# Performance work log

Hardware: AMD Instinct MI355X
Metric: run time of the kernel (lower is better)

The kernel has to match this reference:

```python
import jax, jax.numpy as jnp
import numpy as np

D_MODEL = 1024
NUM_HEADS = 16
HEAD_DIM = D_MODEL // NUM_HEADS
CLAMP = 1e9


def setup_inputs() -> dict:
    key = jax.random.key(0)
    ks = jax.random.split(key, 5)
    B, S = 2, 2048
    x = jax.random.normal(ks[0], (B, S, D_MODEL), dtype=jnp.float32)
    # causal mask, broadcastable over [B, H, S, S]
    mask = jnp.tril(jnp.ones((S, S), dtype=bool))
    Wqkv = jax.random.normal(ks[1], (D_MODEL, 3 * D_MODEL), dtype=jnp.float32) * (1.0 / np.sqrt(D_MODEL))
    bqkv = jax.random.normal(ks[2], (3 * D_MODEL,), dtype=jnp.float32) * 0.02
    Wo = jax.random.normal(ks[3], (D_MODEL, D_MODEL), dtype=jnp.float32) * (1.0 / np.sqrt(D_MODEL))
    bo = jax.random.normal(ks[4], (D_MODEL,), dtype=jnp.float32) * 0.02
    return {"x": x, "mask": mask, "Wqkv": Wqkv, "bqkv": bqkv, "Wo": Wo, "bo": bo}


def reference(x, mask, Wqkv, bqkv, Wo, bo):
    B, S, _ = x.shape
    qkv = x @ Wqkv + bqkv                               # [B, S, 3*d_model]
    qkv = qkv.reshape(B, S, NUM_HEADS, 3 * HEAD_DIM).transpose(0, 2, 1, 3)  # [B, H, S, 3*hd]
    q, k, v = jnp.split(qkv, 3, axis=-1)                # each [B, H, S, hd]
    scale = 1.0 / np.sqrt(HEAD_DIM)
    scores = jnp.einsum('bhqd,bhkd->bhqk', q, k) * scale  # [B, H, S, S]
    scores = jnp.where(mask, scores, -jnp.inf)
    scores = jnp.clip(scores, -CLAMP, CLAMP)
    attn = jax.nn.softmax(scores, axis=-1)
    values = jnp.einsum('bhqk,bhkd->bhqd', attn, v)     # [B, H, S, hd]
    values = values.transpose(0, 2, 1, 3).reshape(B, S, D_MODEL)
    return values @ Wo + bo
```

## Files before the change

kernel.cpp:

```cpp
#include <hip/hip_runtime.h>
#include <hip/hip_bf16.h>

#define S_LEN 2048
#define NHEAD 16
#define HDIM  64
#define DMODEL 1024

typedef unsigned short u16;
typedef __attribute__((ext_vector_type(8))) short short8;
typedef __attribute__((ext_vector_type(4))) float floatx4;
typedef __attribute__((ext_vector_type(4))) u16 u16x4;

__device__ __forceinline__ u16 f2bf(float f) {
  unsigned u = __builtin_bit_cast(unsigned, f);
  u += 0x7fffu + ((u >> 16) & 1u);
  return (u16)(u >> 16);
}
__device__ __forceinline__ float bf2f(u16 b) {
  unsigned u = ((unsigned)b) << 16;
  return __builtin_bit_cast(float, u);
}
__device__ __forceinline__ void gload_lds16(const void* g, void* l) {
  __builtin_amdgcn_global_load_lds((const __attribute__((address_space(1))) unsigned int*)g,
                                   (__attribute__((address_space(3))) unsigned int*)l,
                                   16, 0, 0);
}
__device__ __forceinline__ int swz(int b) { return b ^ (((b >> 7) & 7) << 4); }

#define MFMA16(a, b, c) __builtin_amdgcn_mfma_f32_16x16x32_bf16(a, b, c, 0, 0, 0)


__global__ __launch_bounds__(256) void k_cast(const float* __restrict__ in,
                                              u16* __restrict__ hi, int n) {
  int i = (blockIdx.x * blockDim.x + threadIdx.x) * 4;
  if (i >= n) return;
  float4 v = *(const float4*)(in + i);
  u16x4 hv = {f2bf(v.x), f2bf(v.y), f2bf(v.z), f2bf(v.w)};
  *(u16x4*)(hi + i) = hv;
}

__global__ void k_transpose(const float* __restrict__ in, u16* __restrict__ oh, int R, int C) {
  __shared__ float t[32][33];
  int c0 = blockIdx.x * 32, r0 = blockIdx.y * 32;
  int tx = threadIdx.x, ty = threadIdx.y;
#pragma unroll
  for (int rr = ty; rr < 32; rr += 8) t[rr][tx] = in[(size_t)(r0 + rr) * C + c0 + tx];
  __syncthreads();
#pragma unroll
  for (int rr = ty; rr < 32; rr += 8) {
    float v = t[tx][rr];
    oh[(size_t)(c0 + rr) * R + r0 + tx] = f2bf(v);
  }
}

__device__ __forceinline__ void gemm_main(const u16* __restrict__ A, const u16* __restrict__ B,
                                          int m0, int n0, floatx4 (&acc)[4][4]) {
  __shared__ __align__(16) u16 sA[2][128 * 32];
  __shared__ __align__(16) u16 sB[2][128 * 32];
  const int tid = threadIdx.x, lane = tid & 63;
  const int wid = tid >> 6, wr = wid >> 1, wc = wid & 1;
  const int cl = lane & 15, hi = lane >> 4;
  const int rmask = ((cl >> 1) & 7) << 4;
  const int aoff = (wr * 4096 + cl * 64 + hi * 16) ^ rmask;
  const int boff = (wc * 4096 + cl * 64 + hi * 16) ^ rmask;
#pragma unroll
  for (int i = 0; i < 4; ++i)
#pragma unroll
    for (int j = 0; j < 4; ++j) acc[i][j] = (floatx4){0.f, 0.f, 0.f, 0.f};

  auto stage = [&](int buf, int kt) {
    int k0 = kt * 32;
#pragma unroll
    for (int it = 0; it < 2; ++it) {
      int p = (it * 256 + tid) * 16;
      int q = swz(p);
      int row = q >> 6, colb = q & 63;
      int base = (it * 256 + (tid & ~63)) * 16;
      gload_lds16((const char*)A + (size_t)(m0 + row) * 2048 + k0 * 2 + colb, (char*)sA[buf] + base);
      gload_lds16((const char*)B + (size_t)(n0 + row) * 2048 + k0 * 2 + colb, (char*)sB[buf] + base);
    }
  };
  stage(0, 0);
  __syncthreads();
  for (int kt = 0; kt < 32; ++kt) {
    int cur = kt & 1;
    if (kt + 1 < 32) stage(cur ^ 1, kt + 1);
    short8 a[4], b[4];
#pragma unroll
    for (int i = 0; i < 4; ++i) {
      a[i] = *(const short8*)((const char*)sA[cur] + aoff + i * 1024);
      b[i] = *(const short8*)((const char*)sB[cur] + boff + i * 1024);
    }
    __builtin_amdgcn_s_setprio(1);
#pragma unroll
    for (int i = 0; i < 4; ++i)
#pragma unroll
      for (int j = 0; j < 4; ++j)
        acc[i][j] = MFMA16(a[i], b[j], acc[i][j]);
    __builtin_amdgcn_s_setprio(0);
    __syncthreads();
  }
}

__device__ __forceinline__ void gemm_main_n64(const u16* __restrict__ A, const u16* __restrict__ B,
                                              int m0, int n0, floatx4 (&acc)[4][2]) {
  __shared__ __align__(16) u16 sA[2][128 * 32];
  __shared__ __align__(16) u16 sB[2][64 * 32];
  const int tid = threadIdx.x, lane = tid & 63;
  const int wid = tid >> 6, wr = wid >> 1, wc = wid & 1;
  const int cl = lane & 15, hi = lane >> 4;
  const int rmask = ((cl >> 1) & 7) << 4;
  const int aoff = (wr * 4096 + cl * 64 + hi * 16) ^ rmask;
  const int boff = (wc * 2048 + cl * 64 + hi * 16) ^ rmask;
#pragma unroll
  for (int i = 0; i < 4; ++i)
#pragma unroll
    for (int j = 0; j < 2; ++j) acc[i][j] = (floatx4){0.f, 0.f, 0.f, 0.f};

  auto stage = [&](int buf, int kt) {
    int k0 = kt * 32;
#pragma unroll
    for (int it = 0; it < 2; ++it) {
      int p = (it * 256 + tid) * 16;
      int q = swz(p);
      int row = q >> 6, colb = q & 63;
      int base = (it * 256 + (tid & ~63)) * 16;
      gload_lds16((const char*)A + (size_t)(m0 + row) * 2048 + k0 * 2 + colb, (char*)sA[buf] + base);
    }
    {
      int p = tid * 16;
      int q = swz(p);
      int row = q >> 6, colb = q & 63;
      int base = (tid & ~63) * 16;
      gload_lds16((const char*)B + (size_t)(n0 + row) * 2048 + k0 * 2 + colb, (char*)sB[buf] + base);
    }
  };
  stage(0, 0);
  __syncthreads();
  for (int kt = 0; kt < 32; ++kt) {
    int cur = kt & 1;
    if (kt + 1 < 32) stage(cur ^ 1, kt + 1);
    short8 a[4], b[2];
#pragma unroll
    for (int i = 0; i < 4; ++i)
      a[i] = *(const short8*)((const char*)sA[cur] + aoff + i * 1024);
#pragma unroll
    for (int j = 0; j < 2; ++j)
      b[j] = *(const short8*)((const char*)sB[cur] + boff + j * 1024);
    __builtin_amdgcn_s_setprio(1);
#pragma unroll
    for (int i = 0; i < 4; ++i)
#pragma unroll
      for (int j = 0; j < 2; ++j)
        acc[i][j] = MFMA16(a[i], b[j], acc[i][j]);
    __builtin_amdgcn_s_setprio(0);
    __syncthreads();
  }
}

__global__ __launch_bounds__(256) void k_qkv_gemm(const u16* __restrict__ xh,
                                                  const u16* __restrict__ wh,
                                                  const float* __restrict__ bqkv,
                                                  u16* __restrict__ Qb, u16* __restrict__ Kb,
                                                  u16* __restrict__ Vt) {
  int bid = blockIdx.y * 24 + blockIdx.x;
  int sid = (bid & 7) * 96 + (bid >> 3);
  int m0 = (sid / 24) * 128, n0 = (sid % 24) * 128;
  floatx4 acc[4][4];
  gemm_main(xh, wh, m0, n0, acc);
  const int lane = threadIdx.x & 63, wid = threadIdx.x >> 6;
  const int wr = wid >> 1, wc = wid & 1;
#pragma unroll
  for (int j = 0; j < 4; ++j) {
    int n = n0 + wc * 64 + j * 16 + (lane & 15);
    float bias = bqkv[n];
    int h = n / 192;
    int rr = n - h * 192;
#pragma unroll
    for (int i = 0; i < 4; ++i) {
#pragma unroll
      for (int r = 0; r < 4; ++r) {
        int m = m0 + wr * 64 + i * 16 + (lane >> 4) * 4 + r;
        int b = m >> 11, s = m & 2047;
        float v = acc[i][j][r] + bias;
        u16 bv = f2bf(v);
        int bh = b * 16 + h;
        if (rr < 64)
          Qb[((size_t)bh * 2048 + s) * 64 + rr] = bv;
        else if (rr < 128)
          Kb[((size_t)bh * 2048 + s) * 64 + (rr - 64)] = bv;
        else
          Vt[((size_t)bh * 64 + (rr - 128)) * 2048 + s] = bv;
      }
    }
  }
}

__global__ __launch_bounds__(512, 6) void k_attn(const u16* __restrict__ Qb,
                                                 const u16* __restrict__ Kb,
                                                 const u16* __restrict__ Vt,
                                                 u16* __restrict__ ao,
                                                 u16* __restrict__ pO,
                                                 float* __restrict__ pL) {
  const int bid = blockIdx.x;
  const int bh = (bid & 7) + 8 * ((bid >> 3) / 40);
  const int idx = (bid >> 3) % 40;
  int qt, c;
  if (idx < 4)        { qt = idx;                   c = 0; }
  else if (idx < 12)  { qt = 4 + ((idx - 4) >> 1);  c = (idx - 4) & 1; }
  else if (idx < 24)  { qt = 8 + (idx - 12) / 3;    c = (idx - 12) % 3; }
  else                { qt = 12 + ((idx - 24) >> 2); c = (idx - 24) & 3; }
  const int q0 = qt * 128;
  const int tid = threadIdx.x, lane = tid & 63, wid = tid >> 6;
  const int cl = lane & 15, hi = lane >> 4;
  const int wq0 = q0 + wid * 16;
  const int myq = wq0 + cl;
  const u16* Qp = Qb + (size_t)bh * (S_LEN * HDIM);
  const u16* Kp = Kb + (size_t)bh * (S_LEN * HDIM);
  const u16* Vp = Vt + (size_t)bh * (HDIM * S_LEN);

  __shared__ __align__(16) u16 Kl[2][64 * 64];
  __shared__ __align__(16) u16 Vl[2][64 * 64];
  __shared__ __align__(16) u16 Pl[8][16 * 72];

  const int kvo0 = (cl * 128 + hi * 16) ^ ((cl & 7) << 4);
  const int kvo1 = kvo0 ^ 64;

  short8 qf[2];
#pragma unroll
  for (int kf = 0; kf < 2; ++kf)
    qf[kf] = *(const short8*)&Qp[(size_t)myq * 64 + kf * 32 + hi * 8];

  floatx4 o[4];
#pragma unroll
  for (int fc = 0; fc < 4; ++fc) o[fc] = (floatx4){0.f, 0.f, 0.f, 0.f};
  float lrun = 0.f;

  const int t0 = c * 8;
  const int NTb = min(t0 + 8, 2 * qt + 2);
  const int NTw = 2 * qt + 1 + (wid >> 2);
  const float C1 = 0.125f * 1.44269504f;
  const float C2 = 16.0f * 1.44269504f;

  auto stage = [&](int buf, int kv0) {
    int p = tid * 16;
    int q = swz(p);
    int row = q >> 7, colb = q & 127;
    int base = (tid & ~63) * 16;
    gload_lds16((const char*)Kp + (size_t)(kv0 + row) * 128 + colb, (char*)Kl[buf] + base);
    gload_lds16((const char*)Vp + (size_t)row * 4096 + (size_t)kv0 * 2 + colb, (char*)Vl[buf] + base);
  };
  stage(0, t0 * 64);

  for (int t = t0; t < NTb; ++t) {
    int cur = t & 1;
    asm volatile("s_waitcnt vmcnt(0)" ::: "memory");
    __builtin_amdgcn_s_barrier();
    if (t + 1 < NTb) stage(cur ^ 1, (t + 1) * 64);
    if (t < NTw) {
      int kv0 = t * 64;
      floatx4 sc[4];
#pragma unroll
      for (int fc = 0; fc < 4; ++fc) sc[fc] = (floatx4){0.f, 0.f, 0.f, 0.f};
      __builtin_amdgcn_s_setprio(1);
#pragma unroll
      for (int kf = 0; kf < 2; ++kf) {
        const char* kb = (const char*)Kl[cur] + (kf ? kvo1 : kvo0);
        short8 kfv[4];
#pragma unroll
        for (int fc = 0; fc < 4; ++fc)
          kfv[fc] = *(const short8*)(kb + fc * 2048);
#pragma unroll
        for (int fc = 0; fc < 4; ++fc)
          sc[fc] = MFMA16(kfv[fc], qf[kf], sc[fc]);
      }
      __builtin_amdgcn_s_setprio(0);
      auto smax = [&](bool masked) {
        float ls = 0.f;
#pragma unroll
        for (int fc = 0; fc < 4; ++fc) {
          float p0 = exp2f(sc[fc][0] * C1 - C2);
          float p1 = exp2f(sc[fc][1] * C1 - C2);
          float p2 = exp2f(sc[fc][2] * C1 - C2);
          float p3 = exp2f(sc[fc][3] * C1 - C2);
          if (masked) {
            int key = kv0 + fc * 16 + hi * 4;
            p0 = (key + 0 <= myq) ? p0 : 0.f;
            p1 = (key + 1 <= myq) ? p1 : 0.f;
            p2 = (key + 2 <= myq) ? p2 : 0.f;
            p3 = (key + 3 <= myq) ? p3 : 0.f;
          }
          unsigned r0, r1;
          asm("v_cvt_pk_bf16_f32 %0, %1, %2" : "=v"(r0) : "v"(p0), "v"(p1));
          asm("v_cvt_pk_bf16_f32 %0, %1, %2" : "=v"(r1) : "v"(p2), "v"(p3));
          uint2 rr; rr.x = r0; rr.y = r1;
          *(uint2*)((char*)Pl[wid] + cl * 144 + fc * 32 + hi * 8) = rr;
          ls += (p0 + p1) + (p2 + p3);
        }
        lrun += ls;
      };
      if (t == NTw - 1) smax(true); else smax(false);
      __builtin_amdgcn_s_setprio(1);
#pragma unroll
      for (int kf = 0; kf < 2; ++kf) {
        short8 pa = *(const short8*)((const char*)Pl[wid] + cl * 144 + kf * 64 + hi * 16);
        const char* vbp = (const char*)Vl[cur] + (kf ? kvo1 : kvo0);
        short8 vb[4];
#pragma unroll
        for (int fc = 0; fc < 4; ++fc)
          vb[fc] = *(const short8*)(vbp + fc * 2048);
#pragma unroll
        for (int fc = 0; fc < 4; ++fc)
          o[fc] = MFMA16(pa, vb[fc], o[fc]);
      }
      __builtin_amdgcn_s_setprio(0);
    }
  }
  float l = lrun;
  l += __shfl_xor(l, 16);
  l += __shfl_xor(l, 32);
  if (qt < 4) {
    const int b = bh >> 4, h = bh & 15;
#pragma unroll
    for (int j = 0; j < 4; ++j) {
      float inv = 1.f / __shfl(l, hi * 4 + j);
      int q = wq0 + hi * 4 + j;
#pragma unroll
      for (int fc = 0; fc < 4; ++fc) {
        size_t idx2 = ((size_t)b * 2048 + q) * 1024 + h * 64 + fc * 16 + cl;
        ao[idx2] = f2bf(o[fc][j] * inv);
      }
    }
  } else {
    const int slot = (bh * 12 + (qt - 4)) * 4 + c;
    u16* po = pO + (size_t)slot * 8192 + (size_t)wid * 16 * 64;
    if (hi == 0) pL[slot * 128 + wid * 16 + cl] = l;
#pragma unroll
    for (int j = 0; j < 4; ++j) {
      int row = hi * 4 + j;
#pragma unroll
      for (int fc = 0; fc < 4; ++fc)
        po[row * 64 + fc * 16 + cl] = f2bf(o[fc][j]);
    }
  }
}

__global__ __launch_bounds__(256) void k_attn_reduce(const u16* __restrict__ pO,
                                                     const float* __restrict__ pL,
                                                     u16* __restrict__ ao) {
  int e = blockIdx.x * 256 + threadIdx.x;
  int d0 = (e & 15) * 4;
  int row = (e >> 4) & 127;
  int t = e >> 11;
  int qt = 4 + t % 12;
  int bh = t / 12;
  int nch = (2 * qt + 9) >> 3;
  int slot = t * 4;
  size_t obase = (size_t)slot * 8192 + row * 64 + d0;
  float O0 = 0.f, O1 = 0.f, O2 = 0.f, O3 = 0.f, l = 0.f;
  for (int c = 0; c < nch; ++c) {
    u16x4 v = *(const u16x4*)(pO + obase + (size_t)c * 8192);
    O0 += bf2f(v.x); O1 += bf2f(v.y); O2 += bf2f(v.z); O3 += bf2f(v.w);
    l += pL[(slot + c) * 128 + row];
  }
  float inv = 1.f / l;
  u16x4 r = {f2bf(O0 * inv), f2bf(O1 * inv), f2bf(O2 * inv), f2bf(O3 * inv)};
  int b = bh >> 4, h = bh & 15;
  int q = qt * 128 + row;
  *(u16x4*)(ao + ((size_t)b * 2048 + q) * 1024 + h * 64 + d0) = r;
}

__global__ __launch_bounds__(256) void k_out_gemm(const u16* __restrict__ ao,
                                                  const u16* __restrict__ woh,
                                                  const float* __restrict__ bo, float* __restrict__ out) {
  int bid = blockIdx.x;
  int sid = (bid & 7) * 64 + (bid >> 3);
  int m0 = (sid >> 4) * 128, n0 = (sid & 15) * 64;
  floatx4 acc[4][2];
  gemm_main_n64(ao, woh, m0, n0, acc);
  const int lane = threadIdx.x & 63, wid = threadIdx.x >> 6;
  const int wr = wid >> 1, wc = wid & 1;
#pragma unroll
  for (int j = 0; j < 2; ++j) {
    int n = n0 + wc * 32 + j * 16 + (lane & 15);
    float bias = bo[n];
#pragma unroll
    for (int i = 0; i < 4; ++i) {
#pragma unroll
      for (int r = 0; r < 4; ++r) {
        int m = m0 + wr * 64 + i * 16 + (lane >> 4) * 4 + r;
        out[(size_t)m * 1024 + n] = acc[i][j][r] + bias;
      }
    }
  }
}

extern "C" void kernel_launch(void* const* d_in, const int* in_sizes, int n_in,
                              void* d_out, int out_size, void* d_ws, size_t ws_size,
                              hipStream_t stream) {
  (void)in_sizes; (void)n_in; (void)out_size; (void)ws_size;
  const float* x    = (const float*)d_in[0];
  const float* Wqkv = (const float*)d_in[2];
  const float* bqkv = (const float*)d_in[3];
  const float* Wo   = (const float*)d_in[4];
  const float* bo   = (const float*)d_in[5];
  float* out = (float*)d_out;

  u16* p = (u16*)d_ws;
  u16* xh  = p; p += 4194304;
  u16* wh  = p; p += 3145728;
  u16* woh = p; p += 1048576;
  u16* Qb  = p; p += 4194304;
  u16* Kb  = p; p += 4194304;
  u16* Vt  = p; p += 4194304;
  u16* pO  = p; p += 12582912;
  float* pL = (float*)p; p += 393216;
  u16* ao  = xh;

  k_cast<<<4096, 256, 0, stream>>>(x, xh, 4194304);
  k_transpose<<<dim3(96, 32), dim3(32, 8), 0, stream>>>(Wqkv, wh, 1024, 3072);
  k_transpose<<<dim3(32, 32), dim3(32, 8), 0, stream>>>(Wo, woh, 1024, 1024);
  k_qkv_gemm<<<dim3(24, 32), 256, 0, stream>>>(xh, wh, bqkv, Qb, Kb, Vt);
  k_attn<<<1280, 512, 0, stream>>>(Qb, Kb, Vt, ao, pO, pL);
  k_attn_reduce<<<3072, 256, 0, stream>>>(pO, pL, ao);
  k_out_gemm<<<512, 256, 0, stream>>>(ao, woh, bo, out);
}
```

Before: 128.8 us.

## Merge prep kernels and stage QKV epilogue through LDS for vectorized stores

```diff
diff --git a/kernel.cpp b/kernel.cpp
--- a/kernel.cpp
+++ b/kernel.cpp
@@ -29,34 +29,38 @@
 
 #define MFMA16(a, b, c) __builtin_amdgcn_mfma_f32_16x16x32_bf16(a, b, c, 0, 0, 0)
 
-
-__global__ __launch_bounds__(256) void k_cast(const float* __restrict__ in,
-                                              u16* __restrict__ hi, int n) {
-  int i = (blockIdx.x * blockDim.x + threadIdx.x) * 4;
-  if (i >= n) return;
-  float4 v = *(const float4*)(in + i);
-  u16x4 hv = {f2bf(v.x), f2bf(v.y), f2bf(v.z), f2bf(v.w)};
-  *(u16x4*)(hi + i) = hv;
-}
-
-__global__ void k_transpose(const float* __restrict__ in, u16* __restrict__ oh, int R, int C) {
+__global__ __launch_bounds__(256) void k_prep(const float* __restrict__ x,
+                                              const float* __restrict__ Wqkv,
+                                              const float* __restrict__ Wo,
+                                              u16* __restrict__ xh,
+                                              u16* __restrict__ wh,
+                                              u16* __restrict__ woh) {
+  int bid = blockIdx.x, tid = threadIdx.x;
+  if (bid < 4096) {
+    int i = (bid * 256 + tid) * 4;
+    float4 v = *(const float4*)(x + i);
+    u16x4 hv = {f2bf(v.x), f2bf(v.y), f2bf(v.z), f2bf(v.w)};
+    *(u16x4*)(xh + i) = hv;
+    return;
+  }
   __shared__ float t[32][33];
-  int c0 = blockIdx.x * 32, r0 = blockIdx.y * 32;
-  int tx = threadIdx.x, ty = threadIdx.y;
+  const float* in; u16* oh; int C, bx, by;
+  if (bid < 7168) { int b = bid - 4096; in = Wqkv; oh = wh;  C = 3072; bx = b % 96; by = b / 96; }
+  else            { int b = bid - 7168; in = Wo;   oh = woh; C = 1024; bx = b & 31; by = b >> 5; }
+  const int R = 1024;
+  int c0 = bx * 32, r0 = by * 32;
+  int tx = tid & 31, ty = tid >> 5;
 #pragma unroll
   for (int rr = ty; rr < 32; rr += 8) t[rr][tx] = in[(size_t)(r0 + rr) * C + c0 + tx];
   __syncthreads();
 #pragma unroll
-  for (int rr = ty; rr < 32; rr += 8) {
-    float v = t[tx][rr];
-    oh[(size_t)(c0 + rr) * R + r0 + tx] = f2bf(v);
-  }
+  for (int rr = ty; rr < 32; rr += 8)
+    oh[(size_t)(c0 + rr) * R + r0 + tx] = f2bf(t[tx][rr]);
 }
 
 __device__ __forceinline__ void gemm_main(const u16* __restrict__ A, const u16* __restrict__ B,
-                                          int m0, int n0, floatx4 (&acc)[4][4]) {
-  __shared__ __align__(16) u16 sA[2][128 * 32];
-  __shared__ __align__(16) u16 sB[2][128 * 32];
+                                          int m0, int n0, floatx4 (&acc)[4][4],
+                                          u16* sA, u16* sB) {
   const int tid = threadIdx.x, lane = tid & 63;
   const int wid = tid >> 6, wr = wid >> 1, wc = wid & 1;
   const int cl = lane & 15, hi = lane >> 4;
@@ -75,9 +79,9 @@
       int p = (it * 256 + tid) * 16;
       int q = swz(p);
       int row = q >> 6, colb = q & 63;
-      int base = (it * 256 + (tid & ~63)) * 16;
-      gload_lds16((const char*)A + (size_t)(m0 + row) * 2048 + k0 * 2 + colb, (char*)sA[buf] + base);
-      gload_lds16((const char*)B + (size_t)(n0 + row) * 2048 + k0 * 2 + colb, (char*)sB[buf] + base);
+      int base = buf * 8192 + (it * 256 + (tid & ~63)) * 16;
+      gload_lds16((const char*)A + (size_t)(m0 + row) * 2048 + k0 * 2 + colb, (char*)sA + base);
+      gload_lds16((const char*)B + (size_t)(n0 + row) * 2048 + k0 * 2 + colb, (char*)sB + base);
     }
   };
   stage(0, 0);
@@ -88,8 +92,8 @@
     short8 a[4], b[4];
 #pragma unroll
     for (int i = 0; i < 4; ++i) {
-      a[i] = *(const short8*)((const char*)sA[cur] + aoff + i * 1024);
-      b[i] = *(const short8*)((const char*)sB[cur] + boff + i * 1024);
+      a[i] = *(const short8*)((const char*)sA + cur * 8192 + aoff + i * 1024);
+      b[i] = *(const short8*)((const char*)sB + cur * 8192 + boff + i * 1024);
     }
     __builtin_amdgcn_s_setprio(1);
 #pragma unroll
@@ -166,32 +170,53 @@
   int bid = blockIdx.y * 24 + blockIdx.x;
   int sid = (bid & 7) * 96 + (bid >> 3);
   int m0 = (sid / 24) * 128, n0 = (sid % 24) * 128;
+  __shared__ __align__(16) u16 pool[18432];
   floatx4 acc[4][4];
-  gemm_main(xh, wh, m0, n0, acc);
-  const int lane = threadIdx.x & 63, wid = threadIdx.x >> 6;
+  gemm_main(xh, wh, m0, n0, acc, pool, pool + 8192);
+  const int tid = threadIdx.x, lane = tid & 63, wid = tid >> 6;
   const int wr = wid >> 1, wc = wid & 1;
-#pragma unroll
-  for (int j = 0; j < 4; ++j) {
-    int n = n0 + wc * 64 + j * 16 + (lane & 15);
-    float bias = bqkv[n];
-    int h = n / 192;
-    int rr = n - h * 192;
-#pragma unroll
-    for (int i = 0; i < 4; ++i) {
-#pragma unroll
-      for (int r = 0; r < 4; ++r) {
-        int m = m0 + wr * 64 + i * 16 + (lane >> 4) * 4 + r;
-        int b = m >> 11, s = m & 2047;
-        float v = acc[i][j][r] + bias;
-        u16 bv = f2bf(v);
-        int bh = b * 16 + h;
-        if (rr < 64)
-          Qb[((size_t)bh * 2048 + s) * 64 + rr] = bv;
-        else if (rr < 128)
-          Kb[((size_t)bh * 2048 + s) * 64 + (rr - 64)] = bv;
-        else
-          Vt[((size_t)bh * 64 + (rr - 128)) * 2048 + s] = bv;
-      }
+  const int cl = lane & 15, hi = lane >> 4;
+  const int nbase = n0 + wc * 64;
+  const int h = nbase / 192;
+  const int rr0 = nbase - h * 192;
+  const int mb = m0 + wr * 64;
+  const int b = mb >> 11, s0 = mb & 2047;
+  const int bh = b * 16 + h;
+  u16* buf = pool + wid * 4608;
+  float bias[4];
+#pragma unroll
+  for (int j = 0; j < 4; ++j) bias[j] = bqkv[nbase + j * 16 + cl];
+  if (rr0 < 128) {
+#pragma unroll
+    for (int j = 0; j < 4; ++j)
+#pragma unroll
+      for (int i = 0; i < 4; ++i)
+#pragma unroll
+        for (int r = 0; r < 4; ++r)
+          buf[(i * 16 + hi * 4 + r) * 72 + j * 16 + cl] = f2bf(acc[i][j][r] + bias[j]);
+    asm volatile("s_waitcnt lgkmcnt(0)" ::: "memory");
+    u16* dst0 = (rr0 ? Kb : Qb) + ((size_t)bh * 2048 + s0) * 64;
+#pragma unroll
+    for (int k = 0; k < 8; ++k) {
+      int m_l = k * 8 + (lane >> 3);
+      short8 v = *(const short8*)&buf[m_l * 72 + (lane & 7) * 8];
+      *(short8*)(dst0 + (size_t)m_l * 64 + (lane & 7) * 8) = v;
+    }
+  } else {
+#pragma unroll
+    for (int j = 0; j < 4; ++j)
+#pragma unroll
+      for (int i = 0; i < 4; ++i)
+#pragma unroll
+        for (int r = 0; r < 4; ++r)
+          buf[(j * 16 + cl) * 72 + i * 16 + hi * 4 + r] = f2bf(acc[i][j][r] + bias[j]);
+    asm volatile("s_waitcnt lgkmcnt(0)" ::: "memory");
+    u16* dst0 = Vt + (size_t)bh * 64 * 2048 + s0;
+#pragma unroll
+    for (int k = 0; k < 8; ++k) {
+      int nl = k * 8 + (lane >> 3);
+      short8 v = *(const short8*)&buf[nl * 72 + (lane & 7) * 8];
+      *(short8*)(dst0 + (size_t)nl * 2048 + (lane & 7) * 8) = v;
     }
   }
 }
@@ -417,9 +442,7 @@
   float* pL = (float*)p; p += 393216;
   u16* ao  = xh;
 
-  k_cast<<<4096, 256, 0, stream>>>(x, xh, 4194304);
-  k_transpose<<<dim3(96, 32), dim3(32, 8), 0, stream>>>(Wqkv, wh, 1024, 3072);
-  k_transpose<<<dim3(32, 32), dim3(32, 8), 0, stream>>>(Wo, woh, 1024, 1024);
+  k_prep<<<8192, 256, 0, stream>>>(x, Wqkv, Wo, xh, wh, woh);
   k_qkv_gemm<<<dim3(24, 32), 256, 0, stream>>>(xh, wh, bqkv, Qb, Kb, Vt);
   k_attn<<<1280, 512, 0, stream>>>(Qb, Kb, Vt, ao, pO, pL);
   k_attn_reduce<<<3072, 256, 0, stream>>>(pO, pL, ao);
```

Measured after the change: 117.2 us. -9.1%, faster.
